# Kernel tuning notes

Measured on AMD Instinct MI355X. Metric: run time of the kernel, lower is better.

Reference implementation:

```python
import jax, jax.numpy as jnp
import numpy as np

B, T, C = 4, 2048, 1024
N_HEAD = 16
HEAD_DIM = C // N_HEAD


def setup_inputs() -> dict:
    key = jax.random.key(0)
    k1, k2, k3 = jax.random.split(key, 3)
    x = jax.random.normal(k1, (B, T, C), dtype=jnp.float32)
    W_attn = jax.random.normal(k2, (C, 3 * C), dtype=jnp.float32) * (1.0 / np.sqrt(C))
    b_attn = jnp.zeros((3 * C,), dtype=jnp.float32)
    W_proj = jax.random.normal(k3, (C, C), dtype=jnp.float32) * (1.0 / np.sqrt(C))
    b_proj = jnp.zeros((C,), dtype=jnp.float32)
    return {"x": x, "W_attn": W_attn, "b_attn": b_attn, "W_proj": W_proj, "b_proj": b_proj}


def reference(x, W_attn, b_attn, W_proj, b_proj):
    Bx, Tx, Cx = x.shape
    qkv = x @ W_attn + b_attn  # (B,T,3C)
    q, k, v = jnp.split(qkv, 3, axis=-1)
    # (B, n_head, T, head_dim)
    def to_heads(t):
        return t.reshape(Bx, Tx, N_HEAD, HEAD_DIM).transpose(0, 2, 1, 3)
    q, k, v = to_heads(q), to_heads(k), to_heads(v)
    scale = 1.0 / np.sqrt(HEAD_DIM)
    scores = jnp.einsum('bhqd,bhkd->bhqk', q, k) * scale  # (B,H,T,T)
    causal = jnp.tril(jnp.ones((Tx, Tx), dtype=bool))
    scores = jnp.where(causal[None, None, :, :], scores, -jnp.inf)
    probs = jax.nn.softmax(scores, axis=-1)
    attn = jnp.einsum('bhqk,bhkd->bhqd', probs, v)  # (B,H,T,D)
    attn = attn.transpose(0, 2, 1, 3).reshape(Bx, Tx, Cx)
    return attn @ W_proj + b_proj
```

## Files before the change

### kernel.cpp

```cpp
#include <hip/hip_runtime.h>


typedef __attribute__((ext_vector_type(8))) __bf16 bf16x8;
typedef __attribute__((ext_vector_type(4))) float f32x4;
typedef __attribute__((ext_vector_type(4))) short s16x4;

__device__ __forceinline__ float bf2f(unsigned short h) {
    unsigned u = ((unsigned)h) << 16;
    return __builtin_bit_cast(float, u);
}
__device__ __forceinline__ unsigned short f2bf(float f) {
    unsigned u = __builtin_bit_cast(unsigned, f);
    u += 0x7fffu + ((u >> 16) & 1u);
    return (unsigned short)(u >> 16);
}
__device__ __forceinline__ unsigned pack2bf(float a, float b) {
    return (unsigned)f2bf(a) | ((unsigned)f2bf(b) << 16);
}
__device__ __forceinline__ void gload16(const unsigned short* g, unsigned short* l) {
    __builtin_amdgcn_global_load_lds(
        (const __attribute__((address_space(1))) unsigned int*)g,
        (__attribute__((address_space(3))) unsigned int*)l, 16, 0, 0);
}

__global__ void convert_kernel(const float* __restrict__ in, unsigned short* __restrict__ out,
                               long n) {
    long i = ((long)blockIdx.x * blockDim.x + threadIdx.x) * 4;
    if (i >= n) return;
    f32x4 v = *reinterpret_cast<const f32x4*>(&in[i]);
    s16x4 o;
    o[0] = (short)f2bf(v[0]);
    o[1] = (short)f2bf(v[1]);
    o[2] = (short)f2bf(v[2]);
    o[3] = (short)f2bf(v[3]);
    *reinterpret_cast<s16x4*>(&out[i]) = o;
}

__global__ void transpose_kernel(const float* __restrict__ W,
                                 unsigned short* __restrict__ Wt,
                                 int K, int N) {
    __shared__ float t[32][33];
    const int tid = threadIdx.x;
    const int n0 = blockIdx.x * 32, k0 = blockIdx.y * 32;
    const int row = tid >> 3, c4 = (tid & 7) * 4;
    f32x4 v = *reinterpret_cast<const f32x4*>(&W[(size_t)(k0 + row) * N + n0 + c4]);
    t[row][c4 + 0] = v[0];
    t[row][c4 + 1] = v[1];
    t[row][c4 + 2] = v[2];
    t[row][c4 + 3] = v[3];
    __syncthreads();
    s16x4 o;
    o[0] = (short)f2bf(t[c4 + 0][row]);
    o[1] = (short)f2bf(t[c4 + 1][row]);
    o[2] = (short)f2bf(t[c4 + 2][row]);
    o[3] = (short)f2bf(t[c4 + 3][row]);
    *reinterpret_cast<s16x4*>(&Wt[(size_t)(n0 + row) * K + k0 + c4]) = o;
}

template <int MODE>
__global__ __launch_bounds__(256, 2)
void gemm_kernel(const unsigned short* __restrict__ A,
                 const unsigned short* __restrict__ Bt,
                 const float* __restrict__ bias,
                 float* __restrict__ Cout,
                 unsigned short* __restrict__ Qo,
                 unsigned short* __restrict__ Ko,
                 unsigned short* __restrict__ Vto,
                 int M, int N, int Kd) {
    __shared__ unsigned short As[128 * 32];
    __shared__ unsigned short Bs[128 * 32];
    const int tid = threadIdx.x;
    const int wave = tid >> 6, lane = tid & 63;
    const int l15 = lane & 15, lhi = lane >> 4;
    const int wm = wave >> 1, wn = wave & 1;
    const int m0 = blockIdx.x * 128, n0 = blockIdx.y * 128;

    f32x4 acc[4][4];
#pragma unroll
    for (int i = 0; i < 4; i++)
#pragma unroll
        for (int j = 0; j < 4; j++) acc[i][j] = f32x4{0.f, 0.f, 0.f, 0.f};

    const int r0 = tid >> 2, cb = (tid & 3) * 8;
    const unsigned short* Ap = &A[(size_t)(m0 + r0) * Kd + cb];
    const unsigned short* Bp = &Bt[(size_t)(n0 + r0) * Kd + cb];
    unsigned short* AsD0 = &As[tid * 8];
    unsigned short* AsD1 = &As[64 * 32 + tid * 8];
    unsigned short* BsD0 = &Bs[tid * 8];
    unsigned short* BsD1 = &Bs[64 * 32 + tid * 8];
    const size_t K64 = (size_t)64 * Kd;

    for (int k0 = 0; k0 < Kd; k0 += 32) {
        gload16(Ap + k0, AsD0);
        gload16(Ap + K64 + k0, AsD1);
        gload16(Bp + k0, BsD0);
        gload16(Bp + K64 + k0, BsD1);
        __syncthreads();

        bf16x8 af[4], bfr[4];
#pragma unroll
        for (int i = 0; i < 4; i++) {
            af[i]  = *reinterpret_cast<const bf16x8*>(&As[(wm * 64 + i * 16 + l15) * 32 + lhi * 8]);
            bfr[i] = *reinterpret_cast<const bf16x8*>(&Bs[(wn * 64 + i * 16 + l15) * 32 + lhi * 8]);
        }
#pragma unroll
        for (int i = 0; i < 4; i++)
#pragma unroll
            for (int j = 0; j < 4; j++)
                acc[i][j] = __builtin_amdgcn_mfma_f32_16x16x32_bf16(af[i], bfr[j], acc[i][j], 0, 0, 0);
        __syncthreads();
    }

#pragma unroll
    for (int j = 0; j < 4; j++) {
        const int col = n0 + wn * 64 + j * 16 + l15;
        const float bv = bias[col];
#pragma unroll
        for (int i = 0; i < 4; i++) {
            const int rbase = m0 + wm * 64 + i * 16 + lhi * 4;
#pragma unroll
            for (int r = 0; r < 4; r++) {
                const int row = rbase + r;
                const float oval = acc[i][j][r] + bv;
                if (MODE == 0) {
                    Cout[(size_t)row * N + col] = oval;
                } else {
                    const int sel = col >> 10, c1 = col & 1023;
                    const int h = c1 >> 6, d = c1 & 63;
                    const int b = row >> 11, t = row & 2047;
                    if (sel == 0)
                        Qo[(((size_t)(b * 16 + h)) * 2048 + t) * 64 + d] = f2bf(oval * 0.125f);
                    else if (sel == 1)
                        Ko[(((size_t)(b * 16 + h)) * 2048 + t) * 64 + d] = f2bf(oval);
                    else
                        Vto[(((size_t)(b * 16 + h)) * 64 + d) * 2048 + t] = f2bf(oval);
                }
            }
        }
    }
}

__global__ __launch_bounds__(256, 2)
void attn_kernel(const unsigned short* __restrict__ Q,
                 const unsigned short* __restrict__ Kg,
                 const unsigned short* __restrict__ Vt,
                 unsigned short* __restrict__ Aout) {
    __shared__ unsigned int Pl[4][16 * 36];
    const int tid = threadIdx.x, wave = tid >> 6, lane = tid & 63;
    const int l15 = lane & 15, lhi = lane >> 4;
    const int bid = blockIdx.x;
    const int head = bid & 63;
    const int j = bid >> 6;
    const int qb = (j < 4) ? j : (11 - j);
    const int q0w = qb * 256 + wave * 64;
    const unsigned short* Qh = Q + (size_t)head * (2048 * 64);
    const unsigned short* Kh = Kg + (size_t)head * (2048 * 64);
    const unsigned short* Vh = Vt + (size_t)head * (64 * 2048);
    unsigned int* P = &Pl[wave][0];

    bf16x8 qfr[4][2];
#pragma unroll
    for (int qf = 0; qf < 4; qf++)
#pragma unroll
        for (int dh = 0; dh < 2; dh++)
            qfr[qf][dh] = *reinterpret_cast<const bf16x8*>(
                &Qh[(size_t)(q0w + qf * 16 + l15) * 64 + dh * 32 + lhi * 8]);

    f32x4 o[4][4];
#pragma unroll
    for (int df = 0; df < 4; df++)
#pragma unroll
        for (int qf = 0; qf < 4; qf++) o[df][qf] = f32x4{0.f, 0.f, 0.f, 0.f};
    float m[4] = {-1e30f, -1e30f, -1e30f, -1e30f};
    float l[4] = {0.f, 0.f, 0.f, 0.f};

    const int ntiles = (q0w >> 6) + 1;
    for (int t = 0; t < ntiles; ++t) {
        const int kt = t * 64;
        const bool masked = (t == ntiles - 1);
        bf16x8 kfr[4][2], vfr[4][2];
#pragma unroll
        for (int kf = 0; kf < 4; kf++)
#pragma unroll
            for (int dh = 0; dh < 2; dh++)
                kfr[kf][dh] = *reinterpret_cast<const bf16x8*>(
                    &Kh[(size_t)(kt + kf * 16 + l15) * 64 + dh * 32 + lhi * 8]);
#pragma unroll
        for (int df = 0; df < 4; df++)
#pragma unroll
            for (int kc = 0; kc < 2; kc++)
                vfr[df][kc] = *reinterpret_cast<const bf16x8*>(
                    &Vh[(size_t)(df * 16 + l15) * 2048 + kt + kc * 32 + lhi * 8]);

#pragma unroll
        for (int qf = 0; qf < 4; qf++) {
            f32x4 s[4];
#pragma unroll
            for (int kf = 0; kf < 4; kf++) {
                s[kf] = __builtin_amdgcn_mfma_f32_16x16x32_bf16(kfr[kf][0], qfr[qf][0],
                                                                f32x4{0.f, 0.f, 0.f, 0.f}, 0, 0, 0);
                s[kf] = __builtin_amdgcn_mfma_f32_16x16x32_bf16(kfr[kf][1], qfr[qf][1], s[kf], 0, 0, 0);
            }
            if (masked) {
#pragma unroll
                for (int kf = 0; kf < 4; kf++)
#pragma unroll
                    for (int r = 0; r < 4; r++)
                        if (kf * 16 + lhi * 4 + r > qf * 16 + l15) s[kf][r] = -1e30f;
            }
            float tm = s[0][0];
#pragma unroll
            for (int kf = 0; kf < 4; kf++)
#pragma unroll
                for (int r = 0; r < 4; r++) tm = fmaxf(tm, s[kf][r]);
            tm = fmaxf(tm, __shfl_xor(tm, 16));
            tm = fmaxf(tm, __shfl_xor(tm, 32));
            const float mn = fmaxf(m[qf], tm);
            const float corr = __expf(m[qf] - mn);
            m[qf] = mn;
            float rs = 0.f;
#pragma unroll
            for (int kf = 0; kf < 4; kf++)
#pragma unroll
                for (int r = 0; r < 4; r++) {
                    const float p = __expf(s[kf][r] - mn);
                    s[kf][r] = p;
                    rs += p;
                }
            rs += __shfl_xor(rs, 16);
            rs += __shfl_xor(rs, 32);
            l[qf] = l[qf] * corr + rs;
#pragma unroll
            for (int df = 0; df < 4; df++)
#pragma unroll
                for (int r = 0; r < 4; r++) o[df][qf][r] *= corr;

#pragma unroll
            for (int kf = 0; kf < 4; kf++) {
                P[l15 * 36 + kf * 8 + lhi * 2 + 0] = pack2bf(s[kf][0], s[kf][1]);
                P[l15 * 36 + kf * 8 + lhi * 2 + 1] = pack2bf(s[kf][2], s[kf][3]);
            }
            asm volatile("s_waitcnt lgkmcnt(0)" ::: "memory");
            bf16x8 pb0 = *reinterpret_cast<const bf16x8*>(&P[l15 * 36 + 0 * 16 + lhi * 4]);
            bf16x8 pb1 = *reinterpret_cast<const bf16x8*>(&P[l15 * 36 + 1 * 16 + lhi * 4]);
#pragma unroll
            for (int df = 0; df < 4; df++) {
                o[df][qf] = __builtin_amdgcn_mfma_f32_16x16x32_bf16(vfr[df][0], pb0, o[df][qf], 0, 0, 0);
                o[df][qf] = __builtin_amdgcn_mfma_f32_16x16x32_bf16(vfr[df][1], pb1, o[df][qf], 0, 0, 0);
            }
        }
    }

    const int b = head >> 4, h = head & 15;
#pragma unroll
    for (int qf = 0; qf < 4; qf++) {
        const float inv = 1.0f / l[qf];
        unsigned short* op = Aout + ((size_t)(b * 2048 + q0w + qf * 16 + l15)) * 1024 + h * 64;
#pragma unroll
        for (int df = 0; df < 4; df++) {
            *reinterpret_cast<unsigned*>(&op[df * 16 + lhi * 4]) =
                pack2bf(o[df][qf][0] * inv, o[df][qf][1] * inv);
            *reinterpret_cast<unsigned*>(&op[df * 16 + lhi * 4 + 2]) =
                pack2bf(o[df][qf][2] * inv, o[df][qf][3] * inv);
        }
    }
}

extern "C" void kernel_launch(void* const* d_in, const int* in_sizes, int n_in,
                              void* d_out, int out_size, void* d_ws, size_t ws_size,
                              hipStream_t stream) {
    const float* x     = (const float*)d_in[0];
    const float* Wattn = (const float*)d_in[1];
    const float* battn = (const float*)d_in[2];
    const float* Wproj = (const float*)d_in[3];
    const float* bproj = (const float*)d_in[4];
    float* out = (float*)d_out;

    unsigned short* ws = (unsigned short*)d_ws;
    const size_t HS = (size_t)4 * 16 * 2048 * 64;
    unsigned short* Qb  = ws;
    unsigned short* Kb  = Qb + HS;
    unsigned short* Vtb = Kb + HS;
    unsigned short* Ab  = Vtb + HS;
    unsigned short* Wta = Ab + HS;
    unsigned short* Wtp = Wta + (size_t)3072 * 1024;
    unsigned short* xb  = Wtp + (size_t)1024 * 1024;

    convert_kernel<<<8192, 256, 0, stream>>>(x, xb, (long)HS);
    transpose_kernel<<<dim3(96, 32), 256, 0, stream>>>(Wattn, Wta, 1024, 3072);
    transpose_kernel<<<dim3(32, 32), 256, 0, stream>>>(Wproj, Wtp, 1024, 1024);
    gemm_kernel<1><<<dim3(64, 24), 256, 0, stream>>>(xb, Wta, battn, nullptr, Qb, Kb, Vtb,
                                                     8192, 3072, 1024);
    attn_kernel<<<512, 256, 0, stream>>>(Qb, Kb, Vtb, Ab);
    gemm_kernel<0><<<dim3(64, 8), 256, 0, stream>>>(Ab, Wtp, bproj, out, nullptr, nullptr, nullptr,
                                                    8192, 1024, 1024);
}
```

Measured before the change: 223.3 us.

## Double-buffer LDS tiles in the GEMM kernel to overlap loads with MFMA

The GEMM now keeps two shared-memory buffers for the A and B tiles. It issues the global-to-LDS loads for the next K-slice before running the MFMA work on the current one, and the main loop is unrolled by two over the buffers. This aims to hide global load latency behind matrix math, which the single-buffer version exposed at every K step. The cost is double the LDS footprint (32 KB per block), which could limit occupancy under launch_bounds(256,2).

Measured after the change: 218.6 us. -2.1%, faster.

```diff
diff --git a/kernel.cpp b/kernel.cpp
--- a/kernel.cpp
+++ b/kernel.cpp
@@ -67,8 +67,8 @@
                  unsigned short* __restrict__ Ko,
                  unsigned short* __restrict__ Vto,
                  int M, int N, int Kd) {
-    __shared__ unsigned short As[128 * 32];
-    __shared__ unsigned short Bs[128 * 32];
+    __shared__ unsigned short As[2][128 * 32];
+    __shared__ unsigned short Bs[2][128 * 32];
     const int tid = threadIdx.x;
     const int wave = tid >> 6, lane = tid & 63;
     const int l15 = lane & 15, lhi = lane >> 4;
@@ -84,32 +84,40 @@
     const int r0 = tid >> 2, cb = (tid & 3) * 8;
     const unsigned short* Ap = &A[(size_t)(m0 + r0) * Kd + cb];
     const unsigned short* Bp = &Bt[(size_t)(n0 + r0) * Kd + cb];
-    unsigned short* AsD0 = &As[tid * 8];
-    unsigned short* AsD1 = &As[64 * 32 + tid * 8];
-    unsigned short* BsD0 = &Bs[tid * 8];
-    unsigned short* BsD1 = &Bs[64 * 32 + tid * 8];
     const size_t K64 = (size_t)64 * Kd;
 
-    for (int k0 = 0; k0 < Kd; k0 += 32) {
-        gload16(Ap + k0, AsD0);
-        gload16(Ap + K64 + k0, AsD1);
-        gload16(Bp + k0, BsD0);
-        gload16(Bp + K64 + k0, BsD1);
+#define STAGE(buf, k0)                                      \
+    do {                                                    \
+        gload16(Ap + (k0), &As[buf][tid * 8]);              \
+        gload16(Ap + K64 + (k0), &As[buf][64 * 32 + tid * 8]); \
+        gload16(Bp + (k0), &Bs[buf][tid * 8]);              \
+        gload16(Bp + K64 + (k0), &Bs[buf][64 * 32 + tid * 8]); \
+    } while (0)
+
+#define COMPUTE(buf)                                                                         \
+    do {                                                                                     \
+        bf16x8 af[4], bfr[4];                                                                \
+        _Pragma("unroll") for (int i = 0; i < 4; i++) {                                      \
+            af[i]  = *reinterpret_cast<const bf16x8*>(&As[buf][(wm * 64 + i * 16 + l15) * 32 + lhi * 8]); \
+            bfr[i] = *reinterpret_cast<const bf16x8*>(&Bs[buf][(wn * 64 + i * 16 + l15) * 32 + lhi * 8]); \
+        }                                                                                    \
+        _Pragma("unroll") for (int i = 0; i < 4; i++)                                        \
+            _Pragma("unroll") for (int j = 0; j < 4; j++)                                    \
+                acc[i][j] = __builtin_amdgcn_mfma_f32_16x16x32_bf16(af[i], bfr[j], acc[i][j], 0, 0, 0); \
+    } while (0)
+
+    STAGE(0, 0);
+    __syncthreads();
+    for (int k0 = 0; k0 < Kd; k0 += 64) {
+        STAGE(1, k0 + 32);
+        COMPUTE(0);
         __syncthreads();
-
-        bf16x8 af[4], bfr[4];
-#pragma unroll
-        for (int i = 0; i < 4; i++) {
-            af[i]  = *reinterpret_cast<const bf16x8*>(&As[(wm * 64 + i * 16 + l15) * 32 + lhi * 8]);
-            bfr[i] = *reinterpret_cast<const bf16x8*>(&Bs[(wn * 64 + i * 16 + l15) * 32 + lhi * 8]);
-        }
-#pragma unroll
-        for (int i = 0; i < 4; i++)
-#pragma unroll
-            for (int j = 0; j < 4; j++)
-                acc[i][j] = __builtin_amdgcn_mfma_f32_16x16x32_bf16(af[i], bfr[j], acc[i][j], 0, 0, 0);
+        if (k0 + 64 < Kd) STAGE(0, k0 + 64);
+        COMPUTE(1);
         __syncthreads();
     }
+#undef STAGE
+#undef COMPUTE
 
 #pragma unroll
     for (int j = 0; j < 4; j++) {
```

## Double GEMM K-tile to 64 with XOR-swizzled LDS layout

Applied to the files above, without the earlier changes.

The projection GEMM kernel now loads a 64-wide K slice per iteration instead of 32, halving the number of barrier pairs per K loop. The LDS tile layout is XOR-swizzled on the 16-byte column chunk by row index, and the fragment reads apply the same swizzle to avoid LDS bank conflicts. This doubles LDS use per block and adds more registers for fragments, which may affect occupancy at two blocks per CU.

Result: faster. 197.9 us (-11.4%).

```diff
diff --git a/kernel.cpp b/kernel.cpp
--- a/kernel.cpp
+++ b/kernel.cpp
@@ -5,10 +5,6 @@
 typedef __attribute__((ext_vector_type(4))) float f32x4;
 typedef __attribute__((ext_vector_type(4))) short s16x4;
 
-__device__ __forceinline__ float bf2f(unsigned short h) {
-    unsigned u = ((unsigned)h) << 16;
-    return __builtin_bit_cast(float, u);
-}
 __device__ __forceinline__ unsigned short f2bf(float f) {
     unsigned u = __builtin_bit_cast(unsigned, f);
     u += 0x7fffu + ((u >> 16) & 1u);
@@ -67,8 +63,8 @@
                  unsigned short* __restrict__ Ko,
                  unsigned short* __restrict__ Vto,
                  int M, int N, int Kd) {
-    __shared__ unsigned short As[128 * 32];
-    __shared__ unsigned short Bs[128 * 32];
+    __shared__ unsigned short As[128 * 64];
+    __shared__ unsigned short Bs[128 * 64];
     const int tid = threadIdx.x;
     const int wave = tid >> 6, lane = tid & 63;
     const int l15 = lane & 15, lhi = lane >> 4;
@@ -81,33 +77,39 @@
 #pragma unroll
         for (int j = 0; j < 4; j++) acc[i][j] = f32x4{0.f, 0.f, 0.f, 0.f};
 
-    const int r0 = tid >> 2, cb = (tid & 3) * 8;
-    const unsigned short* Ap = &A[(size_t)(m0 + r0) * Kd + cb];
-    const unsigned short* Bp = &Bt[(size_t)(n0 + r0) * Kd + cb];
-    unsigned short* AsD0 = &As[tid * 8];
-    unsigned short* AsD1 = &As[64 * 32 + tid * 8];
-    unsigned short* BsD0 = &Bs[tid * 8];
-    unsigned short* BsD1 = &Bs[64 * 32 + tid * 8];
-    const size_t K64 = (size_t)64 * Kd;
-
-    for (int k0 = 0; k0 < Kd; k0 += 32) {
-        gload16(Ap + k0, AsD0);
-        gload16(Ap + K64 + k0, AsD1);
-        gload16(Bp + k0, BsD0);
-        gload16(Bp + K64 + k0, BsD1);
+    const int r0 = tid >> 3;
+    const int cswz = (((tid & 7) ^ (r0 & 7)) << 3);
+    const unsigned short* Ap = &A[(size_t)(m0 + r0) * Kd + cswz];
+    const unsigned short* Bp = &Bt[(size_t)(n0 + r0) * Kd + cswz];
+    const size_t K32 = (size_t)32 * Kd;
+    const int csw0 = (lhi * 8) ^ ((l15 & 7) << 3);
+
+    for (int k0 = 0; k0 < Kd; k0 += 64) {
+#pragma unroll
+        for (int blk = 0; blk < 4; blk++) {
+            gload16(Ap + blk * K32 + k0, &As[blk * 2048 + tid * 8]);
+            gload16(Bp + blk * K32 + k0, &Bs[blk * 2048 + tid * 8]);
+        }
         __syncthreads();
 
-        bf16x8 af[4], bfr[4];
-#pragma unroll
-        for (int i = 0; i < 4; i++) {
-            af[i]  = *reinterpret_cast<const bf16x8*>(&As[(wm * 64 + i * 16 + l15) * 32 + lhi * 8]);
-            bfr[i] = *reinterpret_cast<const bf16x8*>(&Bs[(wn * 64 + i * 16 + l15) * 32 + lhi * 8]);
-        }
-#pragma unroll
-        for (int i = 0; i < 4; i++)
-#pragma unroll
-            for (int j = 0; j < 4; j++)
-                acc[i][j] = __builtin_amdgcn_mfma_f32_16x16x32_bf16(af[i], bfr[j], acc[i][j], 0, 0, 0);
+        bf16x8 av[2][4], bv[2][4];
+#pragma unroll
+        for (int ks = 0; ks < 2; ks++)
+#pragma unroll
+            for (int i = 0; i < 4; i++) {
+                av[ks][i] = *reinterpret_cast<const bf16x8*>(
+                    &As[(wm * 64 + i * 16 + l15) * 64 + (ks * 32 ^ csw0)]);
+                bv[ks][i] = *reinterpret_cast<const bf16x8*>(
+                    &Bs[(wn * 64 + i * 16 + l15) * 64 + (ks * 32 ^ csw0)]);
+            }
+#pragma unroll
+        for (int ks = 0; ks < 2; ks++)
+#pragma unroll
+            for (int i = 0; i < 4; i++)
+#pragma unroll
+                for (int j = 0; j < 4; j++)
+                    acc[i][j] = __builtin_amdgcn_mfma_f32_16x16x32_bf16(av[ks][i], bv[ks][j],
+                                                                        acc[i][j], 0, 0, 0);
         __syncthreads();
     }
 
```
